# Kernel tuning notes

Measured on AMD Instinct MI355X. Metric: run time of the kernel, lower is better.

## Reference

```python
import jax, jax.numpy as jnp
import numpy as np

B, L, H_IN = 2, 512, 768
E = 256          # hidden_size
N = 12           # num_labels


def setup_inputs() -> dict:
    key = jax.random.key(0)
    ks = jax.random.split(key, 10)
    lim_in = 1.0 / np.sqrt(H_IN)
    lim_e = 1.0 / np.sqrt(E)
    lim_2e = 1.0 / np.sqrt(2 * E)
    return {
        "x":    jax.random.normal(ks[0], (B, L, H_IN), dtype=jnp.float32),
        "sW":   jax.random.uniform(ks[1], (E, H_IN), jnp.float32, -lim_in, lim_in),
        "sb":   jax.random.uniform(ks[2], (E,), jnp.float32, -lim_in, lim_in),
        "tW":   jax.random.uniform(ks[3], (E, H_IN), jnp.float32, -lim_in, lim_in),
        "tb":   jax.random.uniform(ks[4], (E,), jnp.float32, -lim_in, lim_in),
        "f2W":  jax.random.uniform(ks[5], (E, 2 * E), jnp.float32, -lim_2e, lim_2e),
        "f2b":  jax.random.uniform(ks[6], (E,), jnp.float32, -lim_2e, lim_2e),
        "f3W":  jax.random.normal(ks[7], (N, E), dtype=jnp.float32),  # init_weights: normal_
        "f3b":  jax.random.uniform(ks[8], (N,), jnp.float32, -lim_e, lim_e),
        "blW":  jax.random.normal(ks[9], (E * N, E), dtype=jnp.float32),  # bi_linear, no bias
    }


def reference(x, sW, sb, tW, tb, f2W, f2b, f3W, f3b, blW):
    b, l, _ = x.shape
    s = jax.nn.relu(x @ sW.T + sb)  # [B,L,E]
    t = jax.nn.relu(x @ tW.T + tb)  # [B,L,E]
    # biaffine term: key[b,s,e,n] = (s @ blW.T) reshaped, then key @ t^T
    key = (s @ blW.T).reshape(b, l, E, N)             # [B,L,E,N]
    out1 = jnp.einsum('bsen,ble->bsnl', key, t)       # [B,S,N,L]
    # pairwise concat-MLP, decomposed: cat(u,v) @ f2W.T == u@Wu.T + v@Wv.T
    Wu, Wv = f2W[:, :E], f2W[:, E:]
    su = s @ Wu.T                                     # [B,L,E]
    tv = t @ Wv.T                                     # [B,L,E]
    h = jax.nn.relu(su[:, :, None, :] + tv[:, None, :, :] + f2b)  # [B,L,L,E]
    out2 = h @ f3W.T + f3b                            # [B,L,L,N]
    out2 = jnp.transpose(out2, (0, 1, 3, 2))          # [B,L,N,L]
    return out1 + out2
```

## Files before the change

kernel.cpp:

```cpp
#include <hip/hip_runtime.h>
#include <hip/hip_bf16.h>


typedef unsigned short u16;
typedef __attribute__((ext_vector_type(8))) short    s16x8;
typedef __attribute__((ext_vector_type(8))) _Float16 f16x8;
typedef __attribute__((ext_vector_type(4))) float    f32x4;

__device__ inline u16 f2h(float f) { return __builtin_bit_cast(u16, (_Float16)f); }

__device__ inline s16x8 cvt2(float4 a, float4 b) {
    f16x8 h;
    h[0] = (_Float16)a.x; h[1] = (_Float16)a.y; h[2] = (_Float16)a.z; h[3] = (_Float16)a.w;
    h[4] = (_Float16)b.x; h[5] = (_Float16)b.y; h[6] = (_Float16)b.z; h[7] = (_Float16)b.w;
    return __builtin_bit_cast(s16x8, h);
}

__device__ inline f32x4 mfma_f16(s16x8 a, s16x8 b, f32x4 c) {
    return __builtin_amdgcn_mfma_f32_16x16x32_f16(
        __builtin_bit_cast(f16x8, a), __builtin_bit_cast(f16x8, b), c, 0, 0, 0);
}
__device__ inline f32x4 mfma_f16v(f16x8 a, s16x8 b, f32x4 c) {
    return __builtin_amdgcn_mfma_f32_16x16x32_f16(a, __builtin_bit_cast(f16x8, b), c, 0, 0, 0);
}

__global__ __launch_bounds__(256, 2)
void prep_kernel(const float* __restrict__ x, const float* __restrict__ sW,
                 const float* __restrict__ tW, const float* __restrict__ sb,
                 const float* __restrict__ tb, const float* __restrict__ f2W,
                 const float* __restrict__ blW, const float* __restrict__ f3W,
                 u16* __restrict__ STb, u16* __restrict__ blkw, u16* __restrict__ f3wb)
{
    if (blockIdx.x >= 256) {
        int idx = (blockIdx.x - 256) * 256 + threadIdx.x;
        float4 v;
        u16* dst;
        if (idx < 229376) {
            int i4 = idx * 4;
            int r = i4 >> 8, k = i4 & 255;
            const float* src;
            if (r < 3072)      { int n = r >> 8, e = r & 255; src = &blW[(e * 12 + n) * 256 + k]; }
            else if (r < 3328) { src = &f2W[(r - 3072) * 512 + k]; }
            else               { src = &f2W[(r - 3328) * 512 + 256 + k]; }
            v = *(const float4*)src;
            dst = &blkw[i4];
        } else {
            int i4 = (idx - 229376) * 4;
            int row = i4 >> 8, e = i4 & 255;
            if (row < 12) v = *(const float4*)&f3W[row * 256 + e];
            else          v = make_float4(0.f, 0.f, 0.f, 0.f);
            dst = &f3wb[i4];
        }
        ushort4 o;
        o.x = f2h(v.x); o.y = f2h(v.y); o.z = f2h(v.z); o.w = f2h(v.w);
        *(ushort4*)dst = o;
        return;
    }
    __shared__ u16 As[64 * 72];
    __shared__ u16 Bs[32 * 72];
    const int tid = threadIdx.x;
    const int m0 = (blockIdx.x >> 4) * 64, n0 = (blockIdx.x & 15) * 32;
    const int w = tid >> 6, l = tid & 63;
    const int wr = (w >> 1) * 32, wc = (w & 1) * 16;
    const int lr = l & 15, lg = l >> 4;
    const int srow = tid >> 2, kq = tid & 3;

    const float* ap = &x[(size_t)(m0 + srow) * 768 + kq * 16];
    const bool bstg = (tid < 128);
    const float* bp = nullptr;
    if (bstg) {
        int br = n0 + (tid >> 2);
        bp = (br < 256) ? &sW[(size_t)br * 768 + kq * 16]
                        : &tW[(size_t)(br - 256) * 768 + kq * 16];
    }
    float4 ra0 = *(const float4*)(ap + 0),  ra1 = *(const float4*)(ap + 4);
    float4 ra2 = *(const float4*)(ap + 8),  ra3 = *(const float4*)(ap + 12);
    float4 rb0, rb1, rb2, rb3;
    if (bstg) {
        rb0 = *(const float4*)(bp + 0);  rb1 = *(const float4*)(bp + 4);
        rb2 = *(const float4*)(bp + 8);  rb3 = *(const float4*)(bp + 12);
    }

    f32x4 acc[2] = {};
    for (int k0 = 0; k0 < 768; k0 += 64) {
        __syncthreads();
        *(s16x8*)&As[srow * 72 + kq * 16]     = cvt2(ra0, ra1);
        *(s16x8*)&As[srow * 72 + kq * 16 + 8] = cvt2(ra2, ra3);
        if (bstg) {
            *(s16x8*)&Bs[(tid >> 2) * 72 + kq * 16]     = cvt2(rb0, rb1);
            *(s16x8*)&Bs[(tid >> 2) * 72 + kq * 16 + 8] = cvt2(rb2, rb3);
        }
        __syncthreads();
        if (k0 + 64 < 768) {
            ra0 = *(const float4*)(ap + k0 + 64 + 0);  ra1 = *(const float4*)(ap + k0 + 64 + 4);
            ra2 = *(const float4*)(ap + k0 + 64 + 8);  ra3 = *(const float4*)(ap + k0 + 64 + 12);
            if (bstg) {
                rb0 = *(const float4*)(bp + k0 + 64 + 0);  rb1 = *(const float4*)(bp + k0 + 64 + 4);
                rb2 = *(const float4*)(bp + k0 + 64 + 8);  rb3 = *(const float4*)(bp + k0 + 64 + 12);
            }
        }
#pragma unroll
        for (int kk = 0; kk < 64; kk += 32) {
            s16x8 af[2], bf;
            af[0] = *(const s16x8*)&As[(wr      + lr) * 72 + kk + lg * 8];
            af[1] = *(const s16x8*)&As[(wr + 16 + lr) * 72 + kk + lg * 8];
            bf    = *(const s16x8*)&Bs[(wc      + lr) * 72 + kk + lg * 8];
            acc[0] = mfma_f16(af[0], bf, acc[0]);
            acc[1] = mfma_f16(af[1], bf, acc[1]);
        }
    }
#pragma unroll
    for (int fi = 0; fi < 2; ++fi) {
#pragma unroll
        for (int r = 0; r < 4; ++r) {
            int grow = m0 + wr + fi * 16 + lg * 4 + r;
            int gcol = n0 + wc + lr;
            float bias = (gcol < 256) ? sb[gcol] : tb[gcol - 256];
            float v = fmaxf(acc[fi][r] + bias, 0.f);
            STb[(size_t)grow * 512 + gcol] = f2h(v);
        }
    }
}

__global__ __launch_bounds__(256, 4)
void gemm_kst(const u16* __restrict__ STb, const u16* __restrict__ BLKW,
              const float* __restrict__ f2b,
              u16* __restrict__ KEYP, u16* __restrict__ SUp, u16* __restrict__ TVp)
{
    __shared__ u16 As[64 * 72];
    __shared__ u16 Bs[64 * 72];
    const int tid = threadIdx.x;
    const int m0 = blockIdx.y * 64, n0 = blockIdx.x * 64;
    const int w = tid >> 6, l = tid & 63;
    const int wr = (w >> 1) * 32, wc = (w & 1) * 32;
    const int lr = l & 15, lg = l >> 4;
    const int srow = tid >> 2, kq = tid & 3;

    const u16* A = STb + (n0 >= 3328 ? 256 : 0);
    const u16* ap = &A[(size_t)(m0 + srow) * 512];
    const u16* bp = &BLKW[(size_t)(n0 + srow) * 256];
    s16x8 ra0 = *(const s16x8*)&ap[kq * 8];
    s16x8 ra1 = *(const s16x8*)&ap[(kq + 4) * 8];
    s16x8 rb0 = *(const s16x8*)&bp[kq * 8];
    s16x8 rb1 = *(const s16x8*)&bp[(kq + 4) * 8];

    f32x4 acc[2][2] = {};
    for (int k0 = 0; k0 < 256; k0 += 64) {
        __syncthreads();
        *(s16x8*)&As[srow * 72 + kq * 8]       = ra0;
        *(s16x8*)&As[srow * 72 + (kq + 4) * 8] = ra1;
        *(s16x8*)&Bs[srow * 72 + kq * 8]       = rb0;
        *(s16x8*)&Bs[srow * 72 + (kq + 4) * 8] = rb1;
        __syncthreads();
        if (k0 + 64 < 256) {
            ra0 = *(const s16x8*)&ap[k0 + 64 + kq * 8];
            ra1 = *(const s16x8*)&ap[k0 + 64 + (kq + 4) * 8];
            rb0 = *(const s16x8*)&bp[k0 + 64 + kq * 8];
            rb1 = *(const s16x8*)&bp[k0 + 64 + (kq + 4) * 8];
        }
#pragma unroll
        for (int kk = 0; kk < 64; kk += 32) {
            s16x8 af[2], bf[2];
            af[0] = *(const s16x8*)&As[(wr      + lr) * 72 + kk + lg * 8];
            af[1] = *(const s16x8*)&As[(wr + 16 + lr) * 72 + kk + lg * 8];
            bf[0] = *(const s16x8*)&Bs[(wc      + lr) * 72 + kk + lg * 8];
            bf[1] = *(const s16x8*)&Bs[(wc + 16 + lr) * 72 + kk + lg * 8];
#pragma unroll
            for (int fi = 0; fi < 2; ++fi)
#pragma unroll
                for (int fj = 0; fj < 2; ++fj)
                    acc[fi][fj] = mfma_f16(af[fi], bf[fj], acc[fi][fj]);
        }
    }
#pragma unroll
    for (int fi = 0; fi < 2; ++fi) {
#pragma unroll
        for (int fj = 0; fj < 2; ++fj) {
#pragma unroll
            for (int r = 0; r < 4; ++r) {
                int grow = m0 + wr + fi * 16 + lg * 4 + r;
                int gcol = n0 + wc + fj * 16 + lr;
                float v = acc[fi][fj][r];
                if (gcol < 3072) {
                    int n = gcol >> 8, e = gcol & 255;
                    KEYP[(size_t)n * 262144 + (size_t)grow * 256 + e] = f2h(v);
                } else if (gcol < 3328) {
                    SUp[(size_t)grow * 256 + (gcol - 3072)] = f2h(v);
                } else {
                    TVp[(size_t)grow * 256 + (gcol - 3328)] = f2h(v + f2b[gcol - 3328]);
                }
            }
        }
    }
}

__global__ __launch_bounds__(256, 4)
void fused_out(const u16* __restrict__ KEYP, const u16* __restrict__ STb,
               const u16* __restrict__ SUp, const u16* __restrict__ TVp,
               const u16* __restrict__ F3WH, const float* __restrict__ f3b,
               float* __restrict__ out)
{
    __shared__ __align__(16) char smem[30208];
    u16* lds = (u16*)smem;
    const int KEYC = 0, TC = 7680, SUC = 8960, TVC = 9600, F3C = 10880;

    const int tid = threadIdx.x;
    const int w = tid >> 6, l = tid & 63;

    const int lin  = blockIdx.x + (blockIdx.y << 4) + (blockIdx.z << 9);
    const int orig = (lin & 7) * 128 + (lin >> 3);
    const int j0 = (orig & 15) * 32;
    const int i0 = ((orig >> 4) & 31) * 16;
    const int b  = orig >> 9;

    const int lr = l & 15, lg = l >> 4;

    const u16* sb_[5]; int do_[5];
#pragma unroll
    for (int rr = 0; rr < 5; ++rr) {
        int g = tid + 256 * rr;
        const u16* s = nullptr; int d = 0;
        if (g < 768) {
            int n = g >> 6, ii = (g >> 2) & 15, qq = g & 3;
            s = KEYP + (size_t)n * 262144 + (size_t)(b * 512 + i0 + ii) * 256 + qq * 8;
            d = KEYC + (n * 16 + ii) * 40 + qq * 8;
        } else if (g < 896) {
            int q = g - 768, jj = q >> 2, qq = q & 3;
            s = STb + (size_t)(b * 512 + j0 + jj) * 512 + 256 + qq * 8;
            d = TC + jj * 40 + qq * 8;
        } else if (g < 960) {
            int q = g - 896, ii = q >> 2, qq = q & 3;
            s = SUp + (size_t)(b * 512 + i0 + ii) * 256 + qq * 8;
            d = SUC + ii * 40 + qq * 8;
        } else {
            int q = g - 960, jj = q >> 2, qq = q & 3;
            s = TVp + (size_t)(b * 512 + j0 + jj) * 256 + qq * 8;
            d = TVC + jj * 40 + qq * 8;
        }
        sb_[rr] = s; do_[rr] = d;
    }
    const bool v4 = (tid < 64);

#pragma unroll
    for (int rr = 0; rr < 2; ++rr) {
        int g = tid + 256 * rr;
        int row = g >> 5, qq = g & 31;
        *(s16x8*)&lds[F3C + row * 264 + qq * 8] = *(const s16x8*)&F3WH[row * 256 + qq * 8];
    }

    s16x8 st0, st1, st2, st3, st4 = {};
    f32x4 acc1[3][2] = {};
    f32x4 acc2[8]    = {};

    st0 = *(const s16x8*)(sb_[0]);
    st1 = *(const s16x8*)(sb_[1]);
    st2 = *(const s16x8*)(sb_[2]);
    st3 = *(const s16x8*)(sb_[3]);
    if (v4) st4 = *(const s16x8*)(sb_[4]);

    for (int it = 0; it < 8; ++it) {
        const int e0 = it * 32;
        __syncthreads();
        *(s16x8*)&lds[do_[0]] = st0;
        *(s16x8*)&lds[do_[1]] = st1;
        *(s16x8*)&lds[do_[2]] = st2;
        *(s16x8*)&lds[do_[3]] = st3;
        if (v4) *(s16x8*)&lds[do_[4]] = st4;
        __syncthreads();
        if (it < 7) {
            st0 = *(const s16x8*)(sb_[0] + e0 + 32);
            st1 = *(const s16x8*)(sb_[1] + e0 + 32);
            st2 = *(const s16x8*)(sb_[2] + e0 + 32);
            st3 = *(const s16x8*)(sb_[3] + e0 + 32);
            if (v4) st4 = *(const s16x8*)(sb_[4] + e0 + 32);
        }
        s16x8 tf0 = *(const s16x8*)&lds[TC + lr * 40 + lg * 8];
        s16x8 tf1 = *(const s16x8*)&lds[TC + (16 + lr) * 40 + lg * 8];
#pragma unroll
        for (int a = 0; a < 3; ++a) {
            int n = 3 * w + a;
            s16x8 kf = *(const s16x8*)&lds[KEYC + (n * 16 + lr) * 40 + lg * 8];
            acc1[a][0] = mfma_f16(kf, tf0, acc1[a][0]);
            acc1[a][1] = mfma_f16(kf, tf1, acc1[a][1]);
        }
        f16x8 sv = __builtin_bit_cast(f16x8, *(const s16x8*)&lds[SUC + lr * 40 + lg * 8]);
        s16x8 f3fr = *(const s16x8*)&lds[F3C + lr * 264 + e0 + lg * 8];
#pragma unroll
        for (int jj = 0; jj < 8; ++jj) {
            int j = w * 8 + jj;
            f16x8 tv8 = __builtin_bit_cast(f16x8, *(const s16x8*)&lds[TVC + j * 40 + lg * 8]);
            f16x8 hv = sv + tv8;
#pragma unroll
            for (int q = 0; q < 8; ++q)
                hv[q] = hv[q] > (_Float16)0.f ? hv[q] : (_Float16)0.f;
            acc2[jj] = mfma_f16v(hv, f3fr, acc2[jj]);
        }
    }

    __syncthreads();
    float* mg = (float*)smem;
    if (lr < 12) {
#pragma unroll
        for (int r = 0; r < 4; ++r) {
            int i = lg * 4 + r;
            f32x4 v0, v1;
            v0[0] = acc2[0][r]; v0[1] = acc2[1][r]; v0[2] = acc2[2][r]; v0[3] = acc2[3][r];
            v1[0] = acc2[4][r]; v1[1] = acc2[5][r]; v1[2] = acc2[6][r]; v1[3] = acc2[7][r];
            *(f32x4*)&mg[lr * 580 + i * 36 + w * 8]     = v0;
            *(f32x4*)&mg[lr * 580 + i * 36 + w * 8 + 4] = v1;
        }
    }
    __syncthreads();
#pragma unroll
    for (int a = 0; a < 3; ++a) {
        int n = 3 * w + a;
        float fb = f3b[n];
#pragma unroll
        for (int fj = 0; fj < 2; ++fj) {
            int j = fj * 16 + lr;
#pragma unroll
            for (int r = 0; r < 4; ++r) {
                int i = lg * 4 + r;
                float vv = acc1[a][fj][r] + mg[n * 580 + i * 36 + j] + fb;
                out[(((size_t)(b * 512 + i0 + i)) * 12 + n) * 512 + j0 + j] = vv;
            }
        }
    }
}

extern "C" void kernel_launch(void* const* d_in, const int* in_sizes, int n_in,
                              void* d_out, int out_size, void* d_ws, size_t ws_size,
                              hipStream_t stream)
{
    const float* x   = (const float*)d_in[0];
    const float* sW  = (const float*)d_in[1];
    const float* sb  = (const float*)d_in[2];
    const float* tW  = (const float*)d_in[3];
    const float* tb  = (const float*)d_in[4];
    const float* f2W = (const float*)d_in[5];
    const float* f2b = (const float*)d_in[6];
    const float* f3W = (const float*)d_in[7];
    const float* f3b = (const float*)d_in[8];
    const float* blW = (const float*)d_in[9];
    float* out = (float*)d_out;

    char* p = (char*)d_ws;
    u16* STb   = (u16*)p; p += 1048576;
    u16* blkw  = (u16*)p; p += 1835008;
    u16* KEYP  = (u16*)p; p += 6291456;
    u16* SUp   = (u16*)p; p += 524288;
    u16* TVp   = (u16*)p; p += 524288;
    u16* f3wbg = (u16*)p; p += 8192;

    prep_kernel<<<1156, 256, 0, stream>>>(x, sW, tW, sb, tb, f2W, blW, f3W,
                                          STb, blkw, f3wbg);
    gemm_kst<<<dim3(56, 16), 256, 0, stream>>>(STb, blkw, f2b, KEYP, SUp, TVp);
    fused_out<<<dim3(16, 32, 2), 256, 0, stream>>>(KEYP, STb, SUp, TVp, f3wbg, f3b, out);
}
```

Measured before the change: 46.43 us.

## Store key in MFMA fragment order and load it directly to registers

The gemm_kst epilogue now writes the key tensor in an MFMA-fragment-ordered layout. fused_out can then load each wave's key A-fragments straight from global memory into registers, skipping the LDS staging. The remaining T/TV/SU tiles are double-buffered in LDS, so each iteration needs one barrier instead of two, and global loads are prefetched ahead of use. This trades scattered, less coalesced stores in gemm_kst for less LDS traffic, fewer syncs and better latency hiding in the main fused kernel.

```diff
diff --git a/kernel.cpp b/kernel.cpp
--- a/kernel.cpp
+++ b/kernel.cpp
@@ -125,7 +125,7 @@
 __global__ __launch_bounds__(256, 4)
 void gemm_kst(const u16* __restrict__ STb, const u16* __restrict__ BLKW,
               const float* __restrict__ f2b,
-              u16* __restrict__ KEYP, u16* __restrict__ SUp, u16* __restrict__ TVp)
+              u16* __restrict__ KEYF, u16* __restrict__ SUp, u16* __restrict__ TVp)
 {
     __shared__ u16 As[64 * 72];
     __shared__ u16 Bs[64 * 72];
@@ -183,7 +183,9 @@
                 float v = acc[fi][fj][r];
                 if (gcol < 3072) {
                     int n = gcol >> 8, e = gcol & 255;
-                    KEYP[(size_t)n * 262144 + (size_t)grow * 256 + e] = f2h(v);
+                    int g = grow >> 4, li = grow & 15;
+                    int it = e >> 5, sub = (e >> 3) & 3, eo = e & 7;
+                    KEYF[((((size_t)n * 64 + g) * 8 + it) * 64 + sub * 16 + li) * 8 + eo] = f2h(v);
                 } else if (gcol < 3328) {
                     SUp[(size_t)grow * 256 + (gcol - 3072)] = f2h(v);
                 } else {
@@ -195,14 +197,14 @@
 }
 
 __global__ __launch_bounds__(256, 4)
-void fused_out(const u16* __restrict__ KEYP, const u16* __restrict__ STb,
+void fused_out(const u16* __restrict__ KEYF, const u16* __restrict__ STb,
                const u16* __restrict__ SUp, const u16* __restrict__ TVp,
                const u16* __restrict__ F3WH, const float* __restrict__ f3b,
                float* __restrict__ out)
 {
-    __shared__ __align__(16) char smem[30208];
+    __shared__ __align__(16) char smem[27904];
     u16* lds = (u16*)smem;
-    const int KEYC = 0, TC = 7680, SUC = 8960, TVC = 9600, F3C = 10880;
+    const int TC0 = 0, SUC0 = 2560, TVC0 = 3840, F3C = 6400;
 
     const int tid = threadIdx.x;
     const int w = tid >> 6, l = tid & 63;
@@ -215,31 +217,23 @@
 
     const int lr = l & 15, lg = l >> 4;
 
-    const u16* sb_[5]; int do_[5];
-#pragma unroll
-    for (int rr = 0; rr < 5; ++rr) {
-        int g = tid + 256 * rr;
-        const u16* s = nullptr; int d = 0;
-        if (g < 768) {
-            int n = g >> 6, ii = (g >> 2) & 15, qq = g & 3;
-            s = KEYP + (size_t)n * 262144 + (size_t)(b * 512 + i0 + ii) * 256 + qq * 8;
-            d = KEYC + (n * 16 + ii) * 40 + qq * 8;
-        } else if (g < 896) {
-            int q = g - 768, jj = q >> 2, qq = q & 3;
-            s = STb + (size_t)(b * 512 + j0 + jj) * 512 + 256 + qq * 8;
-            d = TC + jj * 40 + qq * 8;
-        } else if (g < 960) {
-            int q = g - 896, ii = q >> 2, qq = q & 3;
-            s = SUp + (size_t)(b * 512 + i0 + ii) * 256 + qq * 8;
-            d = SUC + ii * 40 + qq * 8;
-        } else {
-            int q = g - 960, jj = q >> 2, qq = q & 3;
-            s = TVp + (size_t)(b * 512 + j0 + jj) * 256 + qq * 8;
-            d = TVC + jj * 40 + qq * 8;
-        }
-        sb_[rr] = s; do_[rr] = d;
-    }
-    const bool v4 = (tid < 64);
+    const u16* src1; int d1;
+    if (tid < 128) {
+        int jj = tid >> 2, qq = tid & 3;
+        src1 = STb + (size_t)(b * 512 + j0 + jj) * 512 + 256 + qq * 8;
+        d1 = TC0 + jj * 40 + qq * 8;
+    } else {
+        int q = tid - 128, jj = q >> 2, qq = q & 3;
+        src1 = TVp + (size_t)(b * 512 + j0 + jj) * 256 + qq * 8;
+        d1 = TVC0 + jj * 40 + qq * 8;
+    }
+    const u16* src2 = nullptr; int d2 = 0;
+    const bool has2 = (tid < 64);
+    if (has2) {
+        int ii = tid >> 2, qq = tid & 3;
+        src2 = SUp + (size_t)(b * 512 + i0 + ii) * 256 + qq * 8;
+        d2 = SUC0 + ii * 40 + qq * 8;
+    }
 
 #pragma unroll
     for (int rr = 0; rr < 2; ++rr) {
@@ -248,56 +242,69 @@
         *(s16x8*)&lds[F3C + row * 264 + qq * 8] = *(const s16x8*)&F3WH[row * 256 + qq * 8];
     }
 
-    s16x8 st0, st1, st2, st3, st4 = {};
+    const int gblk = b * 32 + (i0 >> 4);
+    const u16* kfb0 = KEYF + ((size_t)((3 * w + 0) * 64 + gblk) * 8) * 512 + l * 8;
+    const u16* kfb1 = KEYF + ((size_t)((3 * w + 1) * 64 + gblk) * 8) * 512 + l * 8;
+    const u16* kfb2 = KEYF + ((size_t)((3 * w + 2) * 64 + gblk) * 8) * 512 + l * 8;
+
+    s16x8 r1 = *(const s16x8*)src1;
+    s16x8 r2 = {};
+    if (has2) r2 = *(const s16x8*)src2;
+    *(s16x8*)&lds[d1] = r1;
+    if (has2) *(s16x8*)&lds[d2] = r2;
+    s16x8 kf0 = *(const s16x8*)kfb0;
+    s16x8 kf1 = *(const s16x8*)kfb1;
+    s16x8 kf2 = *(const s16x8*)kfb2;
+    r1 = *(const s16x8*)(src1 + 32);
+    if (has2) r2 = *(const s16x8*)(src2 + 32);
+    __syncthreads();
+
     f32x4 acc1[3][2] = {};
     f32x4 acc2[8]    = {};
 
-    st0 = *(const s16x8*)(sb_[0]);
-    st1 = *(const s16x8*)(sb_[1]);
-    st2 = *(const s16x8*)(sb_[2]);
-    st3 = *(const s16x8*)(sb_[3]);
-    if (v4) st4 = *(const s16x8*)(sb_[4]);
-
+#pragma unroll
     for (int it = 0; it < 8; ++it) {
-        const int e0 = it * 32;
-        __syncthreads();
-        *(s16x8*)&lds[do_[0]] = st0;
-        *(s16x8*)&lds[do_[1]] = st1;
-        *(s16x8*)&lds[do_[2]] = st2;
-        *(s16x8*)&lds[do_[3]] = st3;
-        if (v4) *(s16x8*)&lds[do_[4]] = st4;
-        __syncthreads();
+        const int cur = it & 1, nxt = cur ^ 1;
         if (it < 7) {
-            st0 = *(const s16x8*)(sb_[0] + e0 + 32);
-            st1 = *(const s16x8*)(sb_[1] + e0 + 32);
-            st2 = *(const s16x8*)(sb_[2] + e0 + 32);
-            st3 = *(const s16x8*)(sb_[3] + e0 + 32);
-            if (v4) st4 = *(const s16x8*)(sb_[4] + e0 + 32);
-        }
-        s16x8 tf0 = *(const s16x8*)&lds[TC + lr * 40 + lg * 8];
-        s16x8 tf1 = *(const s16x8*)&lds[TC + (16 + lr) * 40 + lg * 8];
-#pragma unroll
-        for (int a = 0; a < 3; ++a) {
-            int n = 3 * w + a;
-            s16x8 kf = *(const s16x8*)&lds[KEYC + (n * 16 + lr) * 40 + lg * 8];
-            acc1[a][0] = mfma_f16(kf, tf0, acc1[a][0]);
-            acc1[a][1] = mfma_f16(kf, tf1, acc1[a][1]);
-        }
-        f16x8 sv = __builtin_bit_cast(f16x8, *(const s16x8*)&lds[SUC + lr * 40 + lg * 8]);
-        s16x8 f3fr = *(const s16x8*)&lds[F3C + lr * 264 + e0 + lg * 8];
+            *(s16x8*)&lds[d1 + nxt * 1280] = r1;
+            if (has2) *(s16x8*)&lds[d2 + nxt * 640] = r2;
+        }
+        s16x8 tf0 = *(const s16x8*)&lds[TC0 + cur * 1280 + lr * 40 + lg * 8];
+        s16x8 tf1 = *(const s16x8*)&lds[TC0 + cur * 1280 + (16 + lr) * 40 + lg * 8];
+        acc1[0][0] = mfma_f16(kf0, tf0, acc1[0][0]);
+        acc1[0][1] = mfma_f16(kf0, tf1, acc1[0][1]);
+        acc1[1][0] = mfma_f16(kf1, tf0, acc1[1][0]);
+        acc1[1][1] = mfma_f16(kf1, tf1, acc1[1][1]);
+        acc1[2][0] = mfma_f16(kf2, tf0, acc1[2][0]);
+        acc1[2][1] = mfma_f16(kf2, tf1, acc1[2][1]);
+        s16x8 nk0, nk1, nk2;
+        if (it < 7) {
+            nk0 = *(const s16x8*)(kfb0 + (it + 1) * 512);
+            nk1 = *(const s16x8*)(kfb1 + (it + 1) * 512);
+            nk2 = *(const s16x8*)(kfb2 + (it + 1) * 512);
+        }
+        f16x8 sv = __builtin_bit_cast(f16x8,
+            *(const s16x8*)&lds[SUC0 + cur * 640 + lr * 40 + lg * 8]);
+        s16x8 f3fr = *(const s16x8*)&lds[F3C + lr * 264 + it * 32 + lg * 8];
 #pragma unroll
         for (int jj = 0; jj < 8; ++jj) {
             int j = w * 8 + jj;
-            f16x8 tv8 = __builtin_bit_cast(f16x8, *(const s16x8*)&lds[TVC + j * 40 + lg * 8]);
+            f16x8 tv8 = __builtin_bit_cast(f16x8,
+                *(const s16x8*)&lds[TVC0 + cur * 1280 + j * 40 + lg * 8]);
             f16x8 hv = sv + tv8;
 #pragma unroll
             for (int q = 0; q < 8; ++q)
                 hv[q] = hv[q] > (_Float16)0.f ? hv[q] : (_Float16)0.f;
             acc2[jj] = mfma_f16v(hv, f3fr, acc2[jj]);
         }
-    }
-
-    __syncthreads();
+        if (it < 6) {
+            r1 = *(const s16x8*)(src1 + (it + 2) * 32);
+            if (has2) r2 = *(const s16x8*)(src2 + (it + 2) * 32);
+        }
+        if (it < 7) { kf0 = nk0; kf1 = nk1; kf2 = nk2; }
+        __syncthreads();
+    }
+
     float* mg = (float*)smem;
     if (lr < 12) {
 #pragma unroll
@@ -347,13 +354,13 @@
     char* p = (char*)d_ws;
     u16* STb   = (u16*)p; p += 1048576;
     u16* blkw  = (u16*)p; p += 1835008;
-    u16* KEYP  = (u16*)p; p += 6291456;
+    u16* KEYF  = (u16*)p; p += 6291456;
     u16* SUp   = (u16*)p; p += 524288;
     u16* TVp   = (u16*)p; p += 524288;
     u16* f3wbg = (u16*)p; p += 8192;
 
     prep_kernel<<<1156, 256, 0, stream>>>(x, sW, tW, sb, tb, f2W, blW, f3W,
                                           STb, blkw, f3wbg);
-    gemm_kst<<<dim3(56, 16), 256, 0, stream>>>(STb, blkw, f2b, KEYP, SUp, TVp);
-    fused_out<<<dim3(16, 32, 2), 256, 0, stream>>>(KEYP, STb, SUp, TVp, f3wbg, f3b, out);
-}
+    gemm_kst<<<dim3(56, 16), 256, 0, stream>>>(STb, blkw, f2b, KEYF, SUp, TVp);
+    fused_out<<<dim3(16, 32, 2), 256, 0, stream>>>(KEYF, STb, SUp, TVp, f3wbg, f3b, out);
+}
```

Measured after the change: 43.48 us. -6.4%, faster.
